# Performance work log

Hardware: AMD Instinct MI355X
Metric: run time of the kernel (lower is better)

The kernel has to match this reference:

```python
import jax, jax.numpy as jnp
import numpy as np

ATTN_MASK_VALUE = -1e10
HEADS, DIM_HEAD, WSZ = 8, 64, 512


def ln(x, scale, eps=1e-5):
    # haiku LayerNorm(create_scale=True, create_offset=False, axis=-1)
    m = x.mean(-1, keepdims=True)
    v = ((x - m) ** 2).mean(-1, keepdims=True)
    return (x - m) / jnp.sqrt(v + eps) * scale


def local_attn(x, ln_s, qkv_w, ow, ob):
    n, _ = x.shape
    w = n // WSZ
    xn = ln(x, ln_s)
    qkv = xn @ qkv_w                                   # [n, 3*h*d]
    q, k, v = jnp.split(qkv, 3, axis=-1)
    resh = lambda t: t.reshape(w, WSZ, HEADS, DIM_HEAD).transpose(2, 0, 1, 3)  # h w n d
    q, k, v = resh(q), resh(k), resh(v)
    def lookback(t):
        t = jnp.pad(t, ((0, 0), (1, 0), (0, 0), (0, 0)))
        return jnp.concatenate((t[:, :-1], t[:, 1:]), axis=2)  # h w 2*wsz d
    k, v = lookback(k), lookback(v)
    sim = jnp.einsum('hwid,hwjd->hwij', q, k) * (DIM_HEAD ** -0.5)
    mask = jnp.tril(jnp.ones((WSZ, 2 * WSZ), dtype=bool), WSZ)
    sim = jnp.where(mask, sim, ATTN_MASK_VALUE)
    attn = jax.nn.softmax(sim, axis=-1)
    out = jnp.einsum('hwij,hwjd->hwid', attn, v)
    out = out.transpose(1, 2, 0, 3).reshape(n, HEADS * DIM_HEAD)
    return out @ ow + ob


def feedforward(x, ln_s, w1, b1, w2, b2):
    xn = ln(x, ln_s)
    return jax.nn.gelu(xn @ w1 + b1) @ w2 + b2


def gmlp(x, ln_s, win, bin_, sln, sw, sb, sow, sob, pow_, pob):
    n = x.shape[0]
    xn = ln(x, ln_s)
    h = jax.nn.gelu(xn @ win + bin_)                   # [n, d_ff]
    xg, gate = jnp.split(h, 2, axis=-1)                # [n, d_ff/2] each
    gate = ln(gate, sln)
    wm = sw * jnp.tril(jnp.ones((n, n), dtype=sw.dtype))
    gate = jnp.einsum('nd,mn->md', gate, wm) + sb      # causal spatial gate
    s = (xg * gate) @ sow + sob
    return s @ pow_ + pob


def forward(tokens, embed, attn_ln, attn_qkv, attn_ow, attn_ob,
            ff_ln, ff_w1, ff_b1, ff_w2, ff_b2,
            g_ln, g_win, g_bin, g_sln, g_sw, g_sb, g_sow, g_sob, g_pow, g_pob,
            fin_ln, head_w, head_b):
    x = embed[tokens]                                  # [n, dim]

    def block(xc, p):
        xc = xc + local_attn(xc, p['al'], p['aq'], p['aw'], p['ab'])
        xc = xc + feedforward(xc, p['fl'], p['f1'], p['fb1'], p['f2'], p['fb2'])
        return xc, None

    attn_params = {'al': attn_ln, 'aq': attn_qkv, 'aw': attn_ow, 'ab': attn_ob,
                   'fl': ff_ln, 'f1': ff_w1, 'fb1': ff_b1, 'f2': ff_w2, 'fb2': ff_b2}
    x, _ = jax.lax.scan(block, x, attn_params)

    def gblock(xc, p):
        xc = xc + gmlp(xc, p['l'], p['wi'], p['bi'], p['sl'], p['sw'], p['sb'],
                       p['so'], p['sob'], p['po'], p['pob'])
        return xc, None

    g_params = {'l': g_ln, 'wi': g_win, 'bi': g_bin, 'sl': g_sln, 'sw': g_sw,
                'sb': g_sb, 'so': g_sow, 'sob': g_sob, 'po': g_pow, 'pob': g_pob}
    x, _ = jax.lax.scan(gblock, x, g_params)

    return ln(x, fin_ln) @ head_w + head_b             # [n, num_tokens]


def setup_inputs() -> dict:
    key = jax.random.key(0)
    ks = jax.random.split(key, 16)
    n, dim, dff, inner, depth, gdepth, vocab = 2048, 1024, 4096, 512, 6, 2, 32
    sc = 0.02
    eps_sgu = 0.001 / n
    return {
        'tokens': jax.random.randint(ks[0], (n,), 0, vocab),
        'embed': jax.random.normal(ks[1], (vocab, dim)) * sc,
        'attn_ln': jnp.ones((depth, dim)),
        'attn_qkv': jax.random.normal(ks[2], (depth, dim, 3 * inner)) * sc,
        'attn_ow': jax.random.normal(ks[3], (depth, inner, dim)) * sc,
        'attn_ob': jnp.zeros((depth, dim)),
        'ff_ln': jnp.ones((depth, dim)),
        'ff_w1': jax.random.normal(ks[4], (depth, dim, dff)) * sc,
        'ff_b1': jnp.zeros((depth, dff)),
        'ff_w2': jax.random.normal(ks[5], (depth, dff, dim)) * sc,
        'ff_b2': jnp.zeros((depth, dim)),
        'g_ln': jnp.ones((gdepth, dim)),
        'g_win': jax.random.normal(ks[6], (gdepth, dim, dff)) * sc,
        'g_bin': jnp.zeros((gdepth, dff)),
        'g_sln': jnp.ones((gdepth, dff // 2)),
        'g_sw': jax.random.uniform(ks[7], (gdepth, n, n), minval=-eps_sgu, maxval=eps_sgu),
        'g_sb': jnp.ones((gdepth, n, 1)),
        'g_sow': jax.random.normal(ks[8], (gdepth, dff // 2, dff // 2)) * sc,
        'g_sob': jnp.zeros((gdepth, dff // 2)),
        'g_pow': jax.random.normal(ks[9], (gdepth, dff // 2, dim)) * sc,
        'g_pob': jnp.zeros((gdepth, dim)),
        'fin_ln': jnp.ones((dim,)),
        'head_w': jax.random.normal(ks[10], (dim, vocab)) * sc,
        'head_b': jnp.zeros((vocab,)),
    }


def reference(tokens, embed, attn_ln, attn_qkv, attn_ow, attn_ob,
              ff_ln, ff_w1, ff_b1, ff_w2, ff_b2,
              g_ln, g_win, g_bin, g_sln, g_sw, g_sb, g_sow, g_sob, g_pow, g_pob,
              fin_ln, head_w, head_b):
    return forward(tokens, embed, attn_ln, attn_qkv, attn_ow, attn_ob,
                   ff_ln, ff_w1, ff_b1, ff_w2, ff_b2,
                   g_ln, g_win, g_bin, g_sln, g_sw, g_sb, g_sow, g_sob, g_pow, g_pob,
                   fin_ln, head_w, head_b)
```

## Files before the change

kernel.cpp:

```cpp
#include <hip/hip_runtime.h>
#include <hip/hip_bf16.h>
#include <math.h>

using bf16 = __hip_bfloat16;
typedef __bf16 bf16x8 __attribute__((ext_vector_type(8)));
typedef float f32x4 __attribute__((ext_vector_type(4)));

__device__ __forceinline__ float toF(float v) { return v; }
__device__ __forceinline__ float toF(bf16 v) { return __bfloat162float(v); }

__device__ __forceinline__ float gelu_f(float x) {
  float t = tanhf(0.7978845608028654f * (x + 0.044715f * x * x * x));
  return 0.5f * x * (1.0f + t);
}

__device__ __forceinline__ void gld_lds16(const bf16* g, bf16* l) {
  __builtin_amdgcn_global_load_lds(
      (const __attribute__((address_space(1))) void*)g,
      (__attribute__((address_space(3))) void*)l, 16, 0, 0);
}

__device__ __forceinline__ float block_sum(float v) {
  __shared__ float tmp[8];
  int lane = threadIdx.x & 63, w = threadIdx.x >> 6, nw = blockDim.x >> 6;
#pragma unroll
  for (int o = 32; o > 0; o >>= 1) v += __shfl_down(v, o, 64);
  __syncthreads();
  if (lane == 0) tmp[w] = v;
  __syncthreads();
  float r = 0.f;
  for (int i = 0; i < nw; ++i) r += tmp[i];
  return r;
}

__device__ __forceinline__ float block_max(float v) {
  __shared__ float tmp2[8];
  int lane = threadIdx.x & 63, w = threadIdx.x >> 6, nw = blockDim.x >> 6;
#pragma unroll
  for (int o = 32; o > 0; o >>= 1) v = fmaxf(v, __shfl_down(v, o, 64));
  __syncthreads();
  if (lane == 0) tmp2[w] = v;
  __syncthreads();
  float r = -1e30f;
  for (int i = 0; i < nw; ++i) r = fmaxf(r, tmp2[i]);
  return r;
}

template <int BM, int BN, int EPI>
__launch_bounds__((BM / 64) * (BN / 64) * 64)
__global__ void gemm_bt(const bf16* __restrict__ A, int lda, long sAzh, long sAzw,
                        const bf16* __restrict__ B, int ldb, long sBzh, long sBzw,
                        void* __restrict__ C, int ldc, long sCzh, long sCzw,
                        int M, int N, int K, int zdiv,
                        const float* __restrict__ bias,
                        const float* __restrict__ rowbias,
                        const bf16* __restrict__ mul, int ldmul,
                        float* __restrict__ resid, int trilskip) {
  constexpr int BK = 32;
  constexpr int WM = BM / 64, WN = BN / 64;
  constexpr int NT = WM * WN * 64;
  __shared__ __align__(16) bf16 As[BM * BK];
  __shared__ __align__(16) bf16 Bs[BN * BK];
  const int tid = threadIdx.x;
  const int wave = tid >> 6, lane = tid & 63;
  const int wm = wave / WN, wn = wave % WN;
  const int m0 = blockIdx.y * BM, n0 = blockIdx.x * BN;
  const int z = blockIdx.z;
  const int zh = z / zdiv, zw = z % zdiv;
  A += zh * sAzh + zw * sAzw;
  B += zh * sBzh + zw * sBzw;
  const long coff = zh * sCzh + zw * sCzw;

  f32x4 acc[4][4];
#pragma unroll
  for (int i = 0; i < 4; ++i)
#pragma unroll
    for (int j = 0; j < 4; ++j)
#pragma unroll
      for (int r = 0; r < 4; ++r) acc[i][j][r] = 0.0f;

  const int kmax = trilskip ? ((m0 + BM < K) ? (m0 + BM) : K) : K;
  const int lrow = lane & 15, lk = (lane >> 4) << 3;

  for (int k0 = 0; k0 < kmax; k0 += BK) {
#pragma unroll
    for (int c = 0; c < (BM * BK) / (NT * 8); ++c) {
      int e = (c * NT + tid) << 3;
      int r = e >> 5, kk = e & 31;
      gld_lds16(A + (long)(m0 + r) * lda + (k0 + kk), As + e);
    }
#pragma unroll
    for (int c = 0; c < (BN * BK) / (NT * 8); ++c) {
      int e = (c * NT + tid) << 3;
      int r = e >> 5, kk = e & 31;
      gld_lds16(B + (long)(n0 + r) * ldb + (k0 + kk), Bs + e);
    }
    __syncthreads();
    if (trilskip && (k0 + BK > m0)) {
#pragma unroll
      for (int c = 0; c < (BM * BK) / (NT * 8); ++c) {
        int e = (c * NT + tid) << 3;
        int r = e >> 5, kk = e & 31;
        int m = m0 + r;
#pragma unroll
        for (int q = 0; q < 8; ++q)
          if (k0 + kk + q > m) As[e + q] = __float2bfloat16(0.0f);
      }
      __syncthreads();
    }
    bf16x8 af[4], bg[4];
#pragma unroll
    for (int i = 0; i < 4; ++i)
      af[i] = *(const bf16x8*)(As + (wm * 64 + i * 16 + lrow) * BK + lk);
#pragma unroll
    for (int j = 0; j < 4; ++j)
      bg[j] = *(const bf16x8*)(Bs + (wn * 64 + j * 16 + lrow) * BK + lk);
#pragma unroll
    for (int i = 0; i < 4; ++i)
#pragma unroll
      for (int j = 0; j < 4; ++j)
        acc[i][j] = __builtin_amdgcn_mfma_f32_16x16x32_bf16(af[i], bg[j], acc[i][j], 0, 0, 0);
    __syncthreads();
  }

  const int rbase = m0 + wm * 64 + ((lane >> 4) << 2);
  const int cbase = n0 + wn * 64 + (lane & 15);
#pragma unroll
  for (int i = 0; i < 4; ++i) {
#pragma unroll
    for (int j = 0; j < 4; ++j) {
#pragma unroll
      for (int r = 0; r < 4; ++r) {
        int row = rbase + i * 16 + r;
        int col = cbase + j * 16;
        float v = acc[i][j][r];
        long idx = coff + (long)row * ldc + col;
        if (EPI == 0) {
          if (bias) v += bias[col];
          ((bf16*)C)[idx] = __float2bfloat16(v);
        } else if (EPI == 2) {
          v += bias[col];
          ((bf16*)C)[idx] = __float2bfloat16(gelu_f(v));
        } else if (EPI == 3) {
          v += bias[col];
          resid[idx] += v;
        } else if (EPI == 4) {
          v += rowbias[row];
          v *= __bfloat162float(mul[(long)row * ldmul + col]);
          ((bf16*)C)[idx] = __float2bfloat16(v);
        }
      }
    }
  }
}

__global__ void k_embed(const int* __restrict__ tokens, const float* __restrict__ embed,
                        float* __restrict__ x) {
  int t = blockIdx.x;
  int tok = tokens[t];
  for (int j = threadIdx.x; j < 1024; j += 256)
    x[(long)t * 1024 + j] = embed[(long)tok * 1024 + j];
}

template <typename TIN>
__global__ void k_ln(const TIN* __restrict__ in, int ldin, const float* __restrict__ scale,
                     bf16* __restrict__ out, int ldout, int C) {
  int row = blockIdx.x, tid = threadIdx.x;
  const TIN* p = in + (long)row * ldin;
  float loc[8];
  int nper = C >> 8;
  float s = 0.f;
  for (int c = 0; c < nper; ++c) {
    float v = toF(p[c * 256 + tid]);
    loc[c] = v;
    s += v;
  }
  s = block_sum(s);
  float mean = s / (float)C;
  float s2 = 0.f;
  for (int c = 0; c < nper; ++c) {
    float d = loc[c] - mean;
    s2 += d * d;
  }
  s2 = block_sum(s2);
  float inv = 1.0f / sqrtf(s2 / (float)C + 1e-5f);
  for (int c = 0; c < nper; ++c) {
    int j = c * 256 + tid;
    out[(long)row * ldout + j] = __float2bfloat16((loc[c] - mean) * inv * scale[j]);
  }
}

template <typename TIN>
__global__ void k_transpose(const TIN* __restrict__ in, int ldin, bf16* __restrict__ out,
                            int ldout, int rows, int cols) {
  __shared__ bf16 tile[32][33];
  int c0 = blockIdx.x * 32, r0 = blockIdx.y * 32;
  int tx = threadIdx.x & 31, ty = threadIdx.x >> 5;
#pragma unroll
  for (int j = 0; j < 32; j += 8)
    tile[ty + j][tx] = __float2bfloat16(toF(in[(long)(r0 + ty + j) * ldin + c0 + tx]));
  __syncthreads();
#pragma unroll
  for (int j = 0; j < 32; j += 8)
    out[(long)(c0 + ty + j) * ldout + r0 + tx] = tile[tx][ty + j];
}

__global__ void k_cast(const float* __restrict__ in, bf16* __restrict__ out, long n) {
  long i = (long)blockIdx.x * 256 + threadIdx.x;
  if (i < n) out[i] = __float2bfloat16(in[i]);
}

__global__ void k_packk(const bf16* __restrict__ qkv, bf16* __restrict__ kpad) {
  int idx = blockIdx.x * 256 + threadIdx.x;
  int d = idx & 63, t = (idx >> 6) & 2047, h = idx >> 17;
  kpad[(long)h * 163840 + (512 + t) * 64 + d] = qkv[(long)t * 1536 + 512 + h * 64 + d];
}

__global__ void k_zeropad(bf16* __restrict__ kpad, bf16* __restrict__ vtpad) {
  int idx = blockIdx.x * 256 + threadIdx.x;
  bf16 z = __float2bfloat16(0.0f);
  if (idx < 262144) {
    int h = idx >> 15, off = idx & 32767;
    kpad[(long)h * 163840 + off] = z;
  } else {
    int i = idx - 262144;
    int f = i >> 9, j = i & 511;
    vtpad[(long)f * 2560 + j] = z;
  }
}

__global__ void k_softmax(bf16* __restrict__ SP) {
  int row = blockIdx.x;
  int i = row & 511;
  int limit = i + 513;
  bf16* s = SP + (long)row * 1024;
  int tid = threadIdx.x;
  float v[4];
  float mx = -1e30f;
#pragma unroll
  for (int c = 0; c < 4; ++c) {
    int j = c * 256 + tid;
    float xv = (j < limit) ? __bfloat162float(s[j]) * 0.125f : -1e30f;
    v[c] = xv;
    mx = fmaxf(mx, xv);
  }
  mx = block_max(mx);
  float sum = 0.f;
#pragma unroll
  for (int c = 0; c < 4; ++c) {
    float e = (v[c] <= -1e29f) ? 0.f : expf(v[c] - mx);
    v[c] = e;
    sum += e;
  }
  sum = block_sum(sum);
  float inv = 1.0f / sum;
#pragma unroll
  for (int c = 0; c < 4; ++c) {
    int j = c * 256 + tid;
    s[j] = __float2bfloat16(v[c] * inv);
  }
}

__global__ void k_head(const float* __restrict__ x, const float* __restrict__ sc,
                       const float* __restrict__ w, const float* __restrict__ b,
                       float* __restrict__ out) {
  int row = blockIdx.x, tid = threadIdx.x;
  __shared__ float xn[1024];
  const float* p = x + (long)row * 1024;
  float loc[4];
  float s = 0.f;
#pragma unroll
  for (int c = 0; c < 4; ++c) {
    float v = p[c * 256 + tid];
    loc[c] = v;
    s += v;
  }
  s = block_sum(s);
  float mean = s / 1024.f;
  float s2 = 0.f;
#pragma unroll
  for (int c = 0; c < 4; ++c) {
    float d = loc[c] - mean;
    s2 += d * d;
  }
  s2 = block_sum(s2);
  float inv = 1.0f / sqrtf(s2 / 1024.f + 1e-5f);
#pragma unroll
  for (int c = 0; c < 4; ++c) {
    int j = c * 256 + tid;
    xn[j] = (loc[c] - mean) * inv * sc[j];
  }
  __syncthreads();
  int t = tid & 31, sl = tid >> 5;
  float partial = 0.f;
  for (int kk = 0; kk < 128; ++kk) {
    int k = sl * 128 + kk;
    partial += xn[k] * w[k * 32 + t];
  }
  __shared__ float red[256];
  red[tid] = partial;
  __syncthreads();
  if (tid < 32) {
    float r = 0.f;
    for (int q = 0; q < 8; ++q) r += red[q * 32 + t];
    out[(long)row * 32 + t] = r + b[t];
  }
}

extern "C" void kernel_launch(void* const* d_in, const int* in_sizes, int n_in,
                              void* d_out, int out_size, void* d_ws, size_t ws_size,
                              hipStream_t stream) {
  (void)in_sizes; (void)n_in; (void)out_size; (void)ws_size;
  const int*   tokens   = (const int*)d_in[0];
  const float* embed    = (const float*)d_in[1];
  const float* attn_ln  = (const float*)d_in[2];
  const float* attn_qkv = (const float*)d_in[3];
  const float* attn_ow  = (const float*)d_in[4];
  const float* attn_ob  = (const float*)d_in[5];
  const float* ff_ln    = (const float*)d_in[6];
  const float* ff_w1    = (const float*)d_in[7];
  const float* ff_b1    = (const float*)d_in[8];
  const float* ff_w2    = (const float*)d_in[9];
  const float* ff_b2    = (const float*)d_in[10];
  const float* g_ln     = (const float*)d_in[11];
  const float* g_win    = (const float*)d_in[12];
  const float* g_bin    = (const float*)d_in[13];
  const float* g_sln    = (const float*)d_in[14];
  const float* g_sw     = (const float*)d_in[15];
  const float* g_sb     = (const float*)d_in[16];
  const float* g_sow    = (const float*)d_in[17];
  const float* g_sob    = (const float*)d_in[18];
  const float* g_pow    = (const float*)d_in[19];
  const float* g_pob    = (const float*)d_in[20];
  const float* fin_ln   = (const float*)d_in[21];
  const float* head_w   = (const float*)d_in[22];
  const float* head_b   = (const float*)d_in[23];

  char* ws = (char*)d_ws;
  float* x  = (float*)ws;
  bf16* xn  = (bf16*)(ws + 8388608);
  char* SC  = ws + 12582912;
  bf16* qkv   = (bf16*)SC;
  bf16* kpad  = (bf16*)(SC + 6291456);
  bf16* vtpad = (bf16*)(SC + 8912896);
  bf16* SP    = (bf16*)(SC + 11534336);
  bf16* att   = (bf16*)(SC + 45088768);
  bf16* h      = (bf16*)SC;
  bf16* gateLN = (bf16*)(SC + 16777216);
  bf16* gateT  = (bf16*)(SC + 25165824);
  bf16* prod   = (bf16*)(SC + 33554432);
  bf16* sbuf   = (bf16*)(SC + 41943040);
  bf16* W  = (bf16*)(ws + 62914560);
  bf16* W2 = (bf16*)(ws + 71303168);

  k_embed<<<2048, 256, 0, stream>>>(tokens, embed, x);

  for (int L = 0; L < 6; ++L) {
    const float* qkvw = attn_qkv + (long)L * 1024 * 1536;
    const float* oww  = attn_ow + (long)L * 512 * 1024;
    const float* w1   = ff_w1 + (long)L * 1024 * 4096;
    const float* w2   = ff_w2 + (long)L * 4096 * 1024;

    k_ln<float><<<2048, 256, 0, stream>>>(x, 1024, attn_ln + L * 1024, xn, 1024, 1024);
    k_transpose<float><<<dim3(48, 32), 256, 0, stream>>>(qkvw, 1536, W, 1024, 1024, 1536);
    gemm_bt<128, 128, 0><<<dim3(12, 16, 1), 256, 0, stream>>>(
        xn, 1024, 0, 0, W, 1024, 0, 0, qkv, 1536, 0, 0,
        2048, 1536, 1024, 1, nullptr, nullptr, nullptr, 0, nullptr, 0);

    k_packk<<<4096, 256, 0, stream>>>(qkv, kpad);
    k_zeropad<<<2048, 256, 0, stream>>>(kpad, vtpad);
    k_transpose<bf16><<<dim3(16, 64), 256, 0, stream>>>(qkv + 1024, 1536, vtpad + 512, 2560, 2048, 512);

    gemm_bt<128, 128, 0><<<dim3(8, 4, 32), 256, 0, stream>>>(
        qkv, 1536, 64, 786432, kpad, 64, 163840, 32768, SP, 1024, 2097152, 524288,
        512, 1024, 64, 4, nullptr, nullptr, nullptr, 0, nullptr, 0);
    k_softmax<<<16384, 256, 0, stream>>>(SP);
    gemm_bt<128, 64, 0><<<dim3(1, 4, 32), 128, 0, stream>>>(
        SP, 1024, 2097152, 524288, vtpad, 2560, 163840, 512, att, 512, 64, 262144,
        512, 64, 1024, 4, nullptr, nullptr, nullptr, 0, nullptr, 0);
    k_transpose<float><<<dim3(32, 16), 256, 0, stream>>>(oww, 1024, W, 512, 512, 1024);
    gemm_bt<128, 128, 3><<<dim3(8, 16, 1), 256, 0, stream>>>(
        att, 512, 0, 0, W, 512, 0, 0, nullptr, 1024, 0, 0,
        2048, 1024, 512, 1, attn_ob + L * 1024, nullptr, nullptr, 0, x, 0);

    k_ln<float><<<2048, 256, 0, stream>>>(x, 1024, ff_ln + L * 1024, xn, 1024, 1024);
    k_transpose<float><<<dim3(128, 32), 256, 0, stream>>>(w1, 4096, W, 1024, 1024, 4096);
    gemm_bt<128, 128, 2><<<dim3(32, 16, 1), 256, 0, stream>>>(
        xn, 1024, 0, 0, W, 1024, 0, 0, h, 4096, 0, 0,
        2048, 4096, 1024, 1, ff_b1 + L * 4096, nullptr, nullptr, 0, nullptr, 0);
    k_transpose<float><<<dim3(32, 128), 256, 0, stream>>>(w2, 1024, W, 4096, 4096, 1024);
    gemm_bt<128, 128, 3><<<dim3(8, 16, 1), 256, 0, stream>>>(
        h, 4096, 0, 0, W, 4096, 0, 0, nullptr, 1024, 0, 0,
        2048, 1024, 4096, 1, ff_b2 + L * 1024, nullptr, nullptr, 0, x, 0);
  }

  for (int G = 0; G < 2; ++G) {
    const float* winw = g_win + (long)G * 1024 * 4096;
    const float* soww = g_sow + (long)G * 2048 * 2048;
    const float* poww = g_pow + (long)G * 2048 * 1024;

    k_ln<float><<<2048, 256, 0, stream>>>(x, 1024, g_ln + G * 1024, xn, 1024, 1024);
    k_transpose<float><<<dim3(128, 32), 256, 0, stream>>>(winw, 4096, W, 1024, 1024, 4096);
    gemm_bt<128, 128, 2><<<dim3(32, 16, 1), 256, 0, stream>>>(
        xn, 1024, 0, 0, W, 1024, 0, 0, h, 4096, 0, 0,
        2048, 4096, 1024, 1, g_bin + G * 4096, nullptr, nullptr, 0, nullptr, 0);
    k_ln<bf16><<<2048, 256, 0, stream>>>(h + 2048, 4096, g_sln + G * 2048, gateLN, 2048, 2048);
    k_transpose<bf16><<<dim3(64, 64), 256, 0, stream>>>(gateLN, 2048, gateT, 2048, 2048, 2048);
    k_cast<<<16384, 256, 0, stream>>>(g_sw + (long)G * 2048 * 2048, W2, 4194304L);
    gemm_bt<128, 128, 4><<<dim3(16, 16, 1), 256, 0, stream>>>(
        W2, 2048, 0, 0, gateT, 2048, 0, 0, prod, 2048, 0, 0,
        2048, 2048, 2048, 1, nullptr, g_sb + G * 2048, h, 4096, nullptr, 1);
    k_transpose<float><<<dim3(64, 64), 256, 0, stream>>>(soww, 2048, W, 2048, 2048, 2048);
    gemm_bt<128, 128, 0><<<dim3(16, 16, 1), 256, 0, stream>>>(
        prod, 2048, 0, 0, W, 2048, 0, 0, sbuf, 2048, 0, 0,
        2048, 2048, 2048, 1, g_sob + G * 2048, nullptr, nullptr, 0, nullptr, 0);
    k_transpose<float><<<dim3(32, 64), 256, 0, stream>>>(poww, 1024, W, 2048, 2048, 1024);
    gemm_bt<128, 128, 3><<<dim3(8, 16, 1), 256, 0, stream>>>(
        sbuf, 2048, 0, 0, W, 2048, 0, 0, nullptr, 1024, 0, 0,
        2048, 1024, 2048, 1, g_pob + G * 1024, nullptr, nullptr, 0, x, 0);
  }

  k_head<<<2048, 256, 0, stream>>>(x, fin_ln, head_w, head_b, (float*)d_out);
}
```

Measured before the change: 2.425 ms.

## Add split-K with atomic residual accumulation for output-projection GEMMs

Adds a split-K mode to the GEMM kernel: blockIdx.x encodes both an N tile and a K chunk, and each chunk accumulates its partial product into the fp32 residual with atomicAdd. The bias is added only by the first chunk. It is enabled for the attention output, FF down-projection and gMLP projection GEMMs, which previously launched only 128 blocks and so underfilled the GPU. The cost is extra atomic traffic on the residual and a summation order that is no longer deterministic.

```diff
diff --git a/kernel.cpp b/kernel.cpp
--- a/kernel.cpp
+++ b/kernel.cpp
@@ -55,7 +55,8 @@
                         const float* __restrict__ bias,
                         const float* __restrict__ rowbias,
                         const bf16* __restrict__ mul, int ldmul,
-                        float* __restrict__ resid, int trilskip) {
+                        float* __restrict__ resid, int trilskip,
+                        int nxk, int kchunk) {
   constexpr int BK = 32;
   constexpr int WM = BM / 64, WN = BN / 64;
   constexpr int NT = WM * WN * 64;
@@ -64,7 +65,9 @@
   const int tid = threadIdx.x;
   const int wave = tid >> 6, lane = tid & 63;
   const int wm = wave / WN, wn = wave % WN;
-  const int m0 = blockIdx.y * BM, n0 = blockIdx.x * BN;
+  int bx = blockIdx.x, kc = 0;
+  if (kchunk > 0) { kc = bx / nxk; bx -= kc * nxk; }
+  const int m0 = blockIdx.y * BM, n0 = bx * BN;
   const int z = blockIdx.z;
   const int zh = z / zdiv, zw = z % zdiv;
   A += zh * sAzh + zw * sAzw;
@@ -79,10 +82,13 @@
 #pragma unroll
       for (int r = 0; r < 4; ++r) acc[i][j][r] = 0.0f;
 
-  const int kmax = trilskip ? ((m0 + BM < K) ? (m0 + BM) : K) : K;
+  const int kbeg = (kchunk > 0) ? kc * kchunk : 0;
+  int kend = K;
+  if (kchunk > 0 && kbeg + kchunk < kend) kend = kbeg + kchunk;
+  if (trilskip && m0 + BM < kend) kend = m0 + BM;
   const int lrow = lane & 15, lk = (lane >> 4) << 3;
 
-  for (int k0 = 0; k0 < kmax; k0 += BK) {
+  for (int k0 = kbeg; k0 < kend; k0 += BK) {
 #pragma unroll
     for (int c = 0; c < (BM * BK) / (NT * 8); ++c) {
       int e = (c * NT + tid) << 3;
@@ -142,8 +148,13 @@
           v += bias[col];
           ((bf16*)C)[idx] = __float2bfloat16(gelu_f(v));
         } else if (EPI == 3) {
-          v += bias[col];
-          resid[idx] += v;
+          if (kchunk > 0) {
+            if (kbeg == 0) v += bias[col];
+            atomicAdd(&resid[idx], v);
+          } else {
+            v += bias[col];
+            resid[idx] += v;
+          }
         } else if (EPI == 4) {
           v += rowbias[row];
           v *= __bfloat162float(mul[(long)row * ldmul + col]);
@@ -365,7 +376,7 @@
     k_transpose<float><<<dim3(48, 32), 256, 0, stream>>>(qkvw, 1536, W, 1024, 1024, 1536);
     gemm_bt<128, 128, 0><<<dim3(12, 16, 1), 256, 0, stream>>>(
         xn, 1024, 0, 0, W, 1024, 0, 0, qkv, 1536, 0, 0,
-        2048, 1536, 1024, 1, nullptr, nullptr, nullptr, 0, nullptr, 0);
+        2048, 1536, 1024, 1, nullptr, nullptr, nullptr, 0, nullptr, 0, 0, 0);
 
     k_packk<<<4096, 256, 0, stream>>>(qkv, kpad);
     k_zeropad<<<2048, 256, 0, stream>>>(kpad, vtpad);
@@ -373,25 +384,25 @@
 
     gemm_bt<128, 128, 0><<<dim3(8, 4, 32), 256, 0, stream>>>(
         qkv, 1536, 64, 786432, kpad, 64, 163840, 32768, SP, 1024, 2097152, 524288,
-        512, 1024, 64, 4, nullptr, nullptr, nullptr, 0, nullptr, 0);
+        512, 1024, 64, 4, nullptr, nullptr, nullptr, 0, nullptr, 0, 0, 0);
     k_softmax<<<16384, 256, 0, stream>>>(SP);
     gemm_bt<128, 64, 0><<<dim3(1, 4, 32), 128, 0, stream>>>(
         SP, 1024, 2097152, 524288, vtpad, 2560, 163840, 512, att, 512, 64, 262144,
-        512, 64, 1024, 4, nullptr, nullptr, nullptr, 0, nullptr, 0);
+        512, 64, 1024, 4, nullptr, nullptr, nullptr, 0, nullptr, 0, 0, 0);
     k_transpose<float><<<dim3(32, 16), 256, 0, stream>>>(oww, 1024, W, 512, 512, 1024);
-    gemm_bt<128, 128, 3><<<dim3(8, 16, 1), 256, 0, stream>>>(
+    gemm_bt<128, 128, 3><<<dim3(16, 16, 1), 256, 0, stream>>>(
         att, 512, 0, 0, W, 512, 0, 0, nullptr, 1024, 0, 0,
-        2048, 1024, 512, 1, attn_ob + L * 1024, nullptr, nullptr, 0, x, 0);
+        2048, 1024, 512, 1, attn_ob + L * 1024, nullptr, nullptr, 0, x, 0, 8, 256);
 
     k_ln<float><<<2048, 256, 0, stream>>>(x, 1024, ff_ln + L * 1024, xn, 1024, 1024);
     k_transpose<float><<<dim3(128, 32), 256, 0, stream>>>(w1, 4096, W, 1024, 1024, 4096);
     gemm_bt<128, 128, 2><<<dim3(32, 16, 1), 256, 0, stream>>>(
         xn, 1024, 0, 0, W, 1024, 0, 0, h, 4096, 0, 0,
-        2048, 4096, 1024, 1, ff_b1 + L * 4096, nullptr, nullptr, 0, nullptr, 0);
+        2048, 4096, 1024, 1, ff_b1 + L * 4096, nullptr, nullptr, 0, nullptr, 0, 0, 0);
     k_transpose<float><<<dim3(32, 128), 256, 0, stream>>>(w2, 1024, W, 4096, 4096, 1024);
-    gemm_bt<128, 128, 3><<<dim3(8, 16, 1), 256, 0, stream>>>(
+    gemm_bt<128, 128, 3><<<dim3(32, 16, 1), 256, 0, stream>>>(
         h, 4096, 0, 0, W, 4096, 0, 0, nullptr, 1024, 0, 0,
-        2048, 1024, 4096, 1, ff_b2 + L * 1024, nullptr, nullptr, 0, x, 0);
+        2048, 1024, 4096, 1, ff_b2 + L * 1024, nullptr, nullptr, 0, x, 0, 8, 1024);
   }
 
   for (int G = 0; G < 2; ++G) {
@@ -403,21 +414,21 @@
     k_transpose<float><<<dim3(128, 32), 256, 0, stream>>>(winw, 4096, W, 1024, 1024, 4096);
     gemm_bt<128, 128, 2><<<dim3(32, 16, 1), 256, 0, stream>>>(
         xn, 1024, 0, 0, W, 1024, 0, 0, h, 4096, 0, 0,
-        2048, 4096, 1024, 1, g_bin + G * 4096, nullptr, nullptr, 0, nullptr, 0);
+        2048, 4096, 1024, 1, g_bin + G * 4096, nullptr, nullptr, 0, nullptr, 0, 0, 0);
     k_ln<bf16><<<2048, 256, 0, stream>>>(h + 2048, 4096, g_sln + G * 2048, gateLN, 2048, 2048);
     k_transpose<bf16><<<dim3(64, 64), 256, 0, stream>>>(gateLN, 2048, gateT, 2048, 2048, 2048);
     k_cast<<<16384, 256, 0, stream>>>(g_sw + (long)G * 2048 * 2048, W2, 4194304L);
     gemm_bt<128, 128, 4><<<dim3(16, 16, 1), 256, 0, stream>>>(
         W2, 2048, 0, 0, gateT, 2048, 0, 0, prod, 2048, 0, 0,
-        2048, 2048, 2048, 1, nullptr, g_sb + G * 2048, h, 4096, nullptr, 1);
+        2048, 2048, 2048, 1, nullptr, g_sb + G * 2048, h, 4096, nullptr, 1, 0, 0);
     k_transpose<float><<<dim3(64, 64), 256, 0, stream>>>(soww, 2048, W, 2048, 2048, 2048);
     gemm_bt<128, 128, 0><<<dim3(16, 16, 1), 256, 0, stream>>>(
         prod, 2048, 0, 0, W, 2048, 0, 0, sbuf, 2048, 0, 0,
-        2048, 2048, 2048, 1, g_sob + G * 2048, nullptr, nullptr, 0, nullptr, 0);
+        2048, 2048, 2048, 1, g_sob + G * 2048, nullptr, nullptr, 0, nullptr, 0, 0, 0);
     k_transpose<float><<<dim3(32, 64), 256, 0, stream>>>(poww, 1024, W, 2048, 2048, 1024);
-    gemm_bt<128, 128, 3><<<dim3(8, 16, 1), 256, 0, stream>>>(
+    gemm_bt<128, 128, 3><<<dim3(32, 16, 1), 256, 0, stream>>>(
         sbuf, 2048, 0, 0, W, 2048, 0, 0, nullptr, 1024, 0, 0,
-        2048, 1024, 2048, 1, g_pob + G * 1024, nullptr, nullptr, 0, x, 0);
+        2048, 1024, 2048, 1, g_pob + G * 1024, nullptr, nullptr, 0, x, 0, 8, 512);
   }
 
   k_head<<<2048, 256, 0, stream>>>(x, fin_ln, head_w, head_b, (float*)d_out);
```

Result: faster. 2.350 ms (-3.1%).
